# Optimization experiments

Measured on AMD Instinct MI355X. Metric: run time of the kernel, lower is better.

## Reference

```python
import jax, jax.numpy as jnp
import numpy as np
import itertools

DIMS = (128, 128, 128)
CHANNELS = 8
BATCH = 2_097_152


def setup_inputs() -> dict:
    key = jax.random.key(0)
    k1, k2 = jax.random.split(key)
    unList = jax.random.uniform(k1, (BATCH, len(DIMS)), dtype=jnp.float32)
    table = jax.random.uniform(k2, DIMS + (CHANNELS,), dtype=jnp.float32)  # initScale=1, initMode='R'
    return {"unList": unList, "table": table}


def reference(unList, table):
    # N-D multilinear (bilinear/trilinear) interpolated table lookup.
    dims = table.shape[:-1]
    n = len(dims)
    c = table.shape[-1]
    dims_f = jnp.asarray(dims, jnp.float32)
    # map normalized coords [0,1] onto grid [0, dim-1]
    scaled = jnp.clip(unList, 0.0, 1.0) * (dims_f - 1.0)          # [B, n]
    i0 = jnp.clip(jnp.floor(scaled), 0.0, dims_f - 2.0).astype(jnp.int32)  # lower corner
    frac = scaled - i0.astype(jnp.float32)                        # [B, n] in [0,1]
    # flatten grid for single-axis gathers
    strides = jnp.asarray([int(np.prod(dims[k + 1:])) for k in range(n)], jnp.int32)
    table_flat = table.reshape(-1, c)                             # [prod(dims), C]
    out = jnp.zeros((unList.shape[0], c), table.dtype)
    # loop over the 2^n corners (8 for 3D) -- small static loop
    for corner in itertools.product((0, 1), repeat=n):
        bits = jnp.asarray(corner, jnp.int32)                     # [n]
        flat_idx = ((i0 + bits) * strides).sum(-1)                # [B]
        w = jnp.prod(jnp.where(jnp.asarray(corner, bool), frac, 1.0 - frac), axis=-1)  # [B]
        out = out + w[:, None] * table_flat[flat_idx]             # gather + weighted sum
    return out
```

## Files before the change

kernel.cpp:

```cpp
#include <hip/hip_runtime.h>


#define DIM 128
#define CH 8
#define BINS 128
#define CHUNK 4096
#define PPT 16
#define REC_OFF 4096

__device__ __forceinline__ int key_of(float ux) {
    float sx = fminf(fmaxf(ux, 0.0f), 1.0f) * 127.0f;
    float fx0 = fminf(floorf(sx), 126.0f);
    return (int)fx0;
}

__global__ __launch_bounds__(256) void k_hist(const float* __restrict__ un,
                                              unsigned* __restrict__ hist, int batch) {
    __shared__ unsigned lh[BINS];
    for (int i = threadIdx.x; i < BINS; i += blockDim.x) lh[i] = 0;
    __syncthreads();
    int stride = gridDim.x * blockDim.x;
    for (int i = blockIdx.x * blockDim.x + threadIdx.x; i < batch; i += stride)
        atomicAdd(&lh[key_of(un[3 * i])], 1u);
    __syncthreads();
    for (int i = threadIdx.x; i < BINS; i += blockDim.x)
        if (lh[i]) atomicAdd(&hist[i], lh[i]);
}

__global__ void k_scan(const unsigned* __restrict__ hist,
                       unsigned* __restrict__ base, unsigned* __restrict__ cursor) {
    __shared__ unsigned lh[BINS];
    __shared__ unsigned lb[BINS];
    int t = threadIdx.x;
    if (t < BINS) lh[t] = hist[t];
    __syncthreads();
    if (t == 0) {
        unsigned acc = 0;
        for (int i = 0; i < BINS; ++i) { lb[i] = acc; acc += lh[i]; }
    }
    __syncthreads();
    if (t < BINS) { base[t] = lb[t]; cursor[t] = lb[t]; }
}

__global__ __launch_bounds__(256) void k_scatter(const float* __restrict__ un,
                                                 unsigned* __restrict__ cursor,
                                                 float4* __restrict__ rec, int batch) {
    __shared__ unsigned lh[BINS];
    __shared__ unsigned lbase[BINS];
    int t = threadIdx.x;
    for (int i = t; i < BINS; i += blockDim.x) lh[i] = 0;
    __syncthreads();
    int start = blockIdx.x * CHUNK;
    unsigned kr[PPT];
#pragma unroll
    for (int j = 0; j < PPT; ++j) {
        int i = start + j * 256 + t;
        if (i < batch) {
            int k = key_of(un[3 * i]);
            unsigned r = atomicAdd(&lh[k], 1u);
            kr[j] = (unsigned)k | (r << 8);
        } else kr[j] = 0xFFFFFFFFu;
    }
    __syncthreads();
    for (int i = t; i < BINS; i += blockDim.x)
        lbase[i] = lh[i] ? atomicAdd(&cursor[i], lh[i]) : 0u;
    __syncthreads();
#pragma unroll
    for (int j = 0; j < PPT; ++j) {
        int i = start + j * 256 + t;
        if (i < batch) {
            unsigned k = kr[j] & 0xFFu, r = kr[j] >> 8;
            float ux = un[3 * i], uy = un[3 * i + 1], uz = un[3 * i + 2];
            rec[lbase[k] + r] = make_float4(ux, uy, uz, __uint_as_float((unsigned)i));
        }
    }
}

__global__ __launch_bounds__(256) void k_main(const float4* __restrict__ rec,
                                              const float* __restrict__ table,
                                              float* __restrict__ out, int batch) {
    int per = gridDim.x >> 3;
    int pb = blockIdx.x;
    int lb = (pb & 7) * per + (pb >> 3);

    int t = (int)threadIdx.x;
    int lane = t & 63;
    int wave = t >> 6;
    int p = lane >> 2;
    int q = lane & 3;

    int i = lb * 64 + wave * 16 + p;
    if (i >= batch) return;

    float4 r = rec[i];
    unsigned orig = __float_as_uint(r.w);

    const float dmax = 127.0f, imax = 126.0f;
    float sx = fminf(fmaxf(r.x, 0.0f), 1.0f) * dmax;
    float sy = fminf(fmaxf(r.y, 0.0f), 1.0f) * dmax;
    float sz = fminf(fmaxf(r.z, 0.0f), 1.0f) * dmax;
    float fx0 = fminf(floorf(sx), imax);
    float fy0 = fminf(floorf(sy), imax);
    float fz0 = fminf(floorf(sz), imax);
    int x0 = (int)fx0, y0 = (int)fy0, z0 = (int)fz0;
    float fx = sx - fx0, fy = sy - fy0, fz = sz - fz0;

    float wzq = (q & 2) ? fz : (1.0f - fz);
    float gx = 1.0f - fx, gy = 1.0f - fy;
    float w0 = gx * gy * wzq;
    float w1 = gx * fy * wzq;
    float w2 = fx * gy * wzq;
    float w3 = fx * fy * wzq;

    unsigned off = (unsigned)(((x0 * DIM + y0) * DIM + z0) * 32) + (unsigned)(q << 4);
    const char* tb = (const char*)table;

    float4 v0 = *(const float4*)(tb + off);
    float4 v1 = *(const float4*)(tb + off + 4096u);
    float4 v2 = *(const float4*)(tb + off + 524288u);
    float4 v3 = *(const float4*)(tb + off + 528384u);
    __builtin_amdgcn_sched_barrier(0);

    float4 acc;
    acc.x = w0 * v0.x + w1 * v1.x + w2 * v2.x + w3 * v3.x;
    acc.y = w0 * v0.y + w1 * v1.y + w2 * v2.y + w3 * v3.y;
    acc.z = w0 * v0.z + w1 * v1.z + w2 * v2.z + w3 * v3.z;
    acc.w = w0 * v0.w + w1 * v1.w + w2 * v2.w + w3 * v3.w;

    acc.x += __shfl_xor(acc.x, 2);
    acc.y += __shfl_xor(acc.y, 2);
    acc.z += __shfl_xor(acc.z, 2);
    acc.w += __shfl_xor(acc.w, 2);

    if (q < 2)
        *reinterpret_cast<float4*>(out + (size_t)orig * CH + (q << 2)) = acc;
}

__global__ __launch_bounds__(256) void k_naive(const float* __restrict__ un,
                                               const float* __restrict__ table,
                                               float* __restrict__ out, int batch) {
    int b = blockIdx.x * blockDim.x + threadIdx.x;
    if (b >= batch) return;
    float ux = un[3 * b], uy = un[3 * b + 1], uz = un[3 * b + 2];
    const float dmax = 127.0f, imax = 126.0f;
    float sx = fminf(fmaxf(ux, 0.0f), 1.0f) * dmax;
    float sy = fminf(fmaxf(uy, 0.0f), 1.0f) * dmax;
    float sz = fminf(fmaxf(uz, 0.0f), 1.0f) * dmax;
    float fx0 = fminf(floorf(sx), imax);
    float fy0 = fminf(floorf(sy), imax);
    float fz0 = fminf(floorf(sz), imax);
    int x0 = (int)fx0, y0 = (int)fy0, z0 = (int)fz0;
    float fx = sx - fx0, fy = sy - fy0, fz = sz - fz0;
    float wx[2] = {1.0f - fx, fx};
    float wy[2] = {1.0f - fy, fy};
    float wz0 = 1.0f - fz, wz1 = fz;
    float acc[CH];
#pragma unroll
    for (int c = 0; c < CH; ++c) acc[c] = 0.0f;
#pragma unroll
    for (int bx = 0; bx < 2; ++bx)
#pragma unroll
        for (int by = 0; by < 2; ++by) {
            const float* pp = table + ((size_t)((x0 + bx) * DIM + (y0 + by)) * DIM + z0) * CH;
            float wxy = wx[bx] * wy[by];
            float w0 = wxy * wz0, w1 = wxy * wz1;
            float4 a0 = *reinterpret_cast<const float4*>(pp + 0);
            float4 a1 = *reinterpret_cast<const float4*>(pp + 4);
            float4 b0 = *reinterpret_cast<const float4*>(pp + 8);
            float4 b1 = *reinterpret_cast<const float4*>(pp + 12);
            acc[0] += w0 * a0.x + w1 * b0.x;  acc[1] += w0 * a0.y + w1 * b0.y;
            acc[2] += w0 * a0.z + w1 * b0.z;  acc[3] += w0 * a0.w + w1 * b0.w;
            acc[4] += w0 * a1.x + w1 * b1.x;  acc[5] += w0 * a1.y + w1 * b1.y;
            acc[6] += w0 * a1.z + w1 * b1.z;  acc[7] += w0 * a1.w + w1 * b1.w;
        }
    float4* o = reinterpret_cast<float4*>(out + (size_t)b * CH);
    o[0] = make_float4(acc[0], acc[1], acc[2], acc[3]);
    o[1] = make_float4(acc[4], acc[5], acc[6], acc[7]);
}

extern "C" void kernel_launch(void* const* d_in, const int* in_sizes, int n_in,
                              void* d_out, int out_size, void* d_ws, size_t ws_size,
                              hipStream_t stream) {
    const float* un    = (const float*)d_in[0];
    const float* table = (const float*)d_in[1];
    float* out         = (float*)d_out;
    int batch = in_sizes[0] / 3;

    size_t need = (size_t)REC_OFF + (size_t)batch * 16;
    if (ws_size < need) {
        int grid = (batch + 255) / 256;
        k_naive<<<grid, 256, 0, stream>>>(un, table, out, batch);
        return;
    }

    unsigned* hist   = (unsigned*)d_ws;
    unsigned* base   = (unsigned*)((char*)d_ws + 512);
    unsigned* cursor = (unsigned*)((char*)d_ws + 1024);
    float4*   rec    = (float4*)((char*)d_ws + REC_OFF);

    hipMemsetAsync(d_ws, 0, 1536, stream);
    k_hist<<<512, 256, 0, stream>>>(un, hist, batch);
    k_scan<<<1, 128, 0, stream>>>(hist, base, cursor);
    int nscat = (batch + CHUNK - 1) / CHUNK;
    k_scatter<<<nscat, 256, 0, stream>>>(un, cursor, rec, batch);
    int nmain = (batch + 63) / 64;
    nmain = ((nmain + 7) / 8) * 8;
    k_main<<<nmain, 256, 0, stream>>>(rec, table, out, batch);
}
```

Measured before the change: 112.7 us.

## Sort points by 2D (x,y) cell bins using global atomics

Points are now bucketed by their (x0, y0) cell pair, 16129 bins, instead of x0 alone, so neighbouring work items in the gather kernel touch nearby table rows and get better cache locality. The histogram and scatter now use global atomics directly rather than shared-memory staging, and the scan becomes a 1024-thread parallel scan. The main kernel handles four points per thread group to amortise launch and index work. Global atomics on 16K bins risk contention and serialization, and the scatter no longer keeps points in original order within a bin.

```diff
diff --git a/kernel.cpp b/kernel.cpp
--- a/kernel.cpp
+++ b/kernel.cpp
@@ -3,76 +3,64 @@
 
 #define DIM 128
 #define CH 8
-#define BINS 128
-#define CHUNK 4096
-#define PPT 16
-#define REC_OFF 4096
-
-__device__ __forceinline__ int key_of(float ux) {
+#define BINS2 16129
+#define CUR_OFF 65536
+#define REC_OFF 131072
+
+__device__ __forceinline__ int key2_of(float ux, float uy) {
     float sx = fminf(fmaxf(ux, 0.0f), 1.0f) * 127.0f;
-    float fx0 = fminf(floorf(sx), 126.0f);
-    return (int)fx0;
+    float sy = fminf(fmaxf(uy, 0.0f), 1.0f) * 127.0f;
+    int x0 = (int)fminf(floorf(sx), 126.0f);
+    int y0 = (int)fminf(floorf(sy), 126.0f);
+    return x0 * 127 + y0;
 }
 
 __global__ __launch_bounds__(256) void k_hist(const float* __restrict__ un,
                                               unsigned* __restrict__ hist, int batch) {
-    __shared__ unsigned lh[BINS];
-    for (int i = threadIdx.x; i < BINS; i += blockDim.x) lh[i] = 0;
-    __syncthreads();
     int stride = gridDim.x * blockDim.x;
     for (int i = blockIdx.x * blockDim.x + threadIdx.x; i < batch; i += stride)
-        atomicAdd(&lh[key_of(un[3 * i])], 1u);
+        atomicAdd(&hist[key2_of(un[3 * i], un[3 * i + 1])], 1u);
+}
+
+__global__ __launch_bounds__(1024) void k_scan(const unsigned* __restrict__ hist,
+                                               unsigned* __restrict__ cursor) {
+    __shared__ unsigned s[1024];
+    int t = threadIdx.x;
+    int base = t * 16;
+    unsigned loc[16];
+    unsigned sum = 0;
+#pragma unroll
+    for (int j = 0; j < 16; ++j) {
+        int k = base + j;
+        unsigned h = (k < BINS2) ? hist[k] : 0u;
+        loc[j] = sum;
+        sum += h;
+    }
+    s[t] = sum;
     __syncthreads();
-    for (int i = threadIdx.x; i < BINS; i += blockDim.x)
-        if (lh[i]) atomicAdd(&hist[i], lh[i]);
-}
-
-__global__ void k_scan(const unsigned* __restrict__ hist,
-                       unsigned* __restrict__ base, unsigned* __restrict__ cursor) {
-    __shared__ unsigned lh[BINS];
-    __shared__ unsigned lb[BINS];
-    int t = threadIdx.x;
-    if (t < BINS) lh[t] = hist[t];
-    __syncthreads();
-    if (t == 0) {
-        unsigned acc = 0;
-        for (int i = 0; i < BINS; ++i) { lb[i] = acc; acc += lh[i]; }
-    }
-    __syncthreads();
-    if (t < BINS) { base[t] = lb[t]; cursor[t] = lb[t]; }
+    for (int off = 1; off < 1024; off <<= 1) {
+        unsigned v = (t >= off) ? s[t - off] : 0u;
+        __syncthreads();
+        s[t] += v;
+        __syncthreads();
+    }
+    unsigned excl = s[t] - sum;
+#pragma unroll
+    for (int j = 0; j < 16; ++j) {
+        int k = base + j;
+        if (k < BINS2) cursor[k] = excl + loc[j];
+    }
 }
 
 __global__ __launch_bounds__(256) void k_scatter(const float* __restrict__ un,
                                                  unsigned* __restrict__ cursor,
                                                  float4* __restrict__ rec, int batch) {
-    __shared__ unsigned lh[BINS];
-    __shared__ unsigned lbase[BINS];
-    int t = threadIdx.x;
-    for (int i = t; i < BINS; i += blockDim.x) lh[i] = 0;
-    __syncthreads();
-    int start = blockIdx.x * CHUNK;
-    unsigned kr[PPT];
-#pragma unroll
-    for (int j = 0; j < PPT; ++j) {
-        int i = start + j * 256 + t;
-        if (i < batch) {
-            int k = key_of(un[3 * i]);
-            unsigned r = atomicAdd(&lh[k], 1u);
-            kr[j] = (unsigned)k | (r << 8);
-        } else kr[j] = 0xFFFFFFFFu;
-    }
-    __syncthreads();
-    for (int i = t; i < BINS; i += blockDim.x)
-        lbase[i] = lh[i] ? atomicAdd(&cursor[i], lh[i]) : 0u;
-    __syncthreads();
-#pragma unroll
-    for (int j = 0; j < PPT; ++j) {
-        int i = start + j * 256 + t;
-        if (i < batch) {
-            unsigned k = kr[j] & 0xFFu, r = kr[j] >> 8;
-            float ux = un[3 * i], uy = un[3 * i + 1], uz = un[3 * i + 2];
-            rec[lbase[k] + r] = make_float4(ux, uy, uz, __uint_as_float((unsigned)i));
-        }
+    int stride = gridDim.x * blockDim.x;
+    for (int i = blockIdx.x * blockDim.x + threadIdx.x; i < batch; i += stride) {
+        float ux = un[3 * i], uy = un[3 * i + 1], uz = un[3 * i + 2];
+        int k = key2_of(ux, uy);
+        unsigned r = atomicAdd(&cursor[k], 1u);
+        rec[r] = make_float4(ux, uy, uz, __uint_as_float((unsigned)i));
     }
 }
 
@@ -89,51 +77,56 @@
     int p = lane >> 2;
     int q = lane & 3;
 
-    int i = lb * 64 + wave * 16 + p;
-    if (i >= batch) return;
-
-    float4 r = rec[i];
-    unsigned orig = __float_as_uint(r.w);
-
     const float dmax = 127.0f, imax = 126.0f;
-    float sx = fminf(fmaxf(r.x, 0.0f), 1.0f) * dmax;
-    float sy = fminf(fmaxf(r.y, 0.0f), 1.0f) * dmax;
-    float sz = fminf(fmaxf(r.z, 0.0f), 1.0f) * dmax;
-    float fx0 = fminf(floorf(sx), imax);
-    float fy0 = fminf(floorf(sy), imax);
-    float fz0 = fminf(floorf(sz), imax);
-    int x0 = (int)fx0, y0 = (int)fy0, z0 = (int)fz0;
-    float fx = sx - fx0, fy = sy - fy0, fz = sz - fz0;
-
-    float wzq = (q & 2) ? fz : (1.0f - fz);
-    float gx = 1.0f - fx, gy = 1.0f - fy;
-    float w0 = gx * gy * wzq;
-    float w1 = gx * fy * wzq;
-    float w2 = fx * gy * wzq;
-    float w3 = fx * fy * wzq;
-
-    unsigned off = (unsigned)(((x0 * DIM + y0) * DIM + z0) * 32) + (unsigned)(q << 4);
     const char* tb = (const char*)table;
-
-    float4 v0 = *(const float4*)(tb + off);
-    float4 v1 = *(const float4*)(tb + off + 4096u);
-    float4 v2 = *(const float4*)(tb + off + 524288u);
-    float4 v3 = *(const float4*)(tb + off + 528384u);
-    __builtin_amdgcn_sched_barrier(0);
-
-    float4 acc;
-    acc.x = w0 * v0.x + w1 * v1.x + w2 * v2.x + w3 * v3.x;
-    acc.y = w0 * v0.y + w1 * v1.y + w2 * v2.y + w3 * v3.y;
-    acc.z = w0 * v0.z + w1 * v1.z + w2 * v2.z + w3 * v3.z;
-    acc.w = w0 * v0.w + w1 * v1.w + w2 * v2.w + w3 * v3.w;
-
-    acc.x += __shfl_xor(acc.x, 2);
-    acc.y += __shfl_xor(acc.y, 2);
-    acc.z += __shfl_xor(acc.z, 2);
-    acc.w += __shfl_xor(acc.w, 2);
-
-    if (q < 2)
-        *reinterpret_cast<float4*>(out + (size_t)orig * CH + (q << 2)) = acc;
+    const unsigned qoff = (unsigned)(q << 4);
+
+    int blk = lb * 256 + wave * 16 + p;
+#pragma unroll
+    for (int j = 0; j < 4; ++j) {
+        int i = blk + j * 64;
+        if (i >= batch) continue;
+
+        float4 r = rec[i];
+        unsigned orig = __float_as_uint(r.w);
+
+        float sx = fminf(fmaxf(r.x, 0.0f), 1.0f) * dmax;
+        float sy = fminf(fmaxf(r.y, 0.0f), 1.0f) * dmax;
+        float sz = fminf(fmaxf(r.z, 0.0f), 1.0f) * dmax;
+        float fx0 = fminf(floorf(sx), imax);
+        float fy0 = fminf(floorf(sy), imax);
+        float fz0 = fminf(floorf(sz), imax);
+        int x0 = (int)fx0, y0 = (int)fy0, z0 = (int)fz0;
+        float fx = sx - fx0, fy = sy - fy0, fz = sz - fz0;
+
+        float wzq = (q & 2) ? fz : (1.0f - fz);
+        float gx = 1.0f - fx, gy = 1.0f - fy;
+        float w0 = gx * gy * wzq;
+        float w1 = gx * fy * wzq;
+        float w2 = fx * gy * wzq;
+        float w3 = fx * fy * wzq;
+
+        unsigned off = (unsigned)(((x0 * DIM + y0) * DIM + z0) * 32) + qoff;
+
+        float4 v0 = *(const float4*)(tb + off);
+        float4 v1 = *(const float4*)(tb + off + 4096u);
+        float4 v2 = *(const float4*)(tb + off + 524288u);
+        float4 v3 = *(const float4*)(tb + off + 528384u);
+
+        float4 acc;
+        acc.x = w0 * v0.x + w1 * v1.x + w2 * v2.x + w3 * v3.x;
+        acc.y = w0 * v0.y + w1 * v1.y + w2 * v2.y + w3 * v3.y;
+        acc.z = w0 * v0.z + w1 * v1.z + w2 * v2.z + w3 * v3.z;
+        acc.w = w0 * v0.w + w1 * v1.w + w2 * v2.w + w3 * v3.w;
+
+        acc.x += __shfl_xor(acc.x, 2);
+        acc.y += __shfl_xor(acc.y, 2);
+        acc.z += __shfl_xor(acc.z, 2);
+        acc.w += __shfl_xor(acc.w, 2);
+
+        if (q < 2)
+            *reinterpret_cast<float4*>(out + (size_t)orig * CH + (q << 2)) = acc;
+    }
 }
 
 __global__ __launch_bounds__(256) void k_naive(const float* __restrict__ un,
@@ -194,16 +187,15 @@
     }
 
     unsigned* hist   = (unsigned*)d_ws;
-    unsigned* base   = (unsigned*)((char*)d_ws + 512);
-    unsigned* cursor = (unsigned*)((char*)d_ws + 1024);
+    unsigned* cursor = (unsigned*)((char*)d_ws + CUR_OFF);
     float4*   rec    = (float4*)((char*)d_ws + REC_OFF);
 
-    hipMemsetAsync(d_ws, 0, 1536, stream);
-    k_hist<<<512, 256, 0, stream>>>(un, hist, batch);
-    k_scan<<<1, 128, 0, stream>>>(hist, base, cursor);
-    int nscat = (batch + CHUNK - 1) / CHUNK;
-    k_scatter<<<nscat, 256, 0, stream>>>(un, cursor, rec, batch);
-    int nmain = (batch + 63) / 64;
+    hipMemsetAsync(d_ws, 0, CUR_OFF, stream);
+    k_hist<<<2048, 256, 0, stream>>>(un, hist, batch);
+    k_scan<<<1, 1024, 0, stream>>>(hist, cursor);
+    k_scatter<<<2048, 256, 0, stream>>>(un, cursor, rec, batch);
+
+    int nmain = (batch + 255) / 256;
     nmain = ((nmain + 7) / 8) * 8;
     k_main<<<nmain, 256, 0, stream>>>(rec, table, out, batch);
 }
```

Measured after the change: 303.5 us. +169.3%, slower.
